# Optimization experiments

Measured on AMD Instinct MI355X. Metric: run time of the kernel, lower is better.

Reference implementation:

```python
import jax, jax.numpy as jnp
import numpy as np

B, C, H, W = 8, 256, 128, 128


def setup_inputs() -> dict:
    key = jax.random.key(0)
    ks = jax.random.split(key, 8)
    s = 1.0 / np.sqrt(C)
    return {
        "edge_feature": jax.random.normal(ks[0], (B, C, H, W), jnp.float32),
        "mask_feature": jax.random.normal(ks[1], (B, C, H, W), jnp.float32),
        # 1x1 conv weights [out_dim, in_dim] + biases
        "Wq": jax.random.normal(ks[2], (C, C), jnp.float32) * s,
        "bq": jax.random.normal(ks[3], (C,), jnp.float32) * 0.01,
        "Wk": jax.random.normal(ks[4], (C, C), jnp.float32) * s,
        "bk": jax.random.normal(ks[5], (C,), jnp.float32) * 0.01,
        "Wv": jax.random.normal(ks[6], (C, C), jnp.float32) * s,
        "bv": jax.random.normal(ks[7], (C,), jnp.float32) * 0.01,
        # torch initializes gamma=0; use 0.5 so the attention path is exercised
        "gamma": jnp.array(0.5, jnp.float32),
    }


def _conv1x1(x, w, b):
    # x: [B,C,H,W], w: [O,C] -> [B,O,H,W]
    return jnp.einsum('oc,bchw->bohw', w, x) + b[None, :, None, None]


def reference(edge_feature, mask_feature, Wq, bq, Wk, bk, Wv, bv, gamma):
    b, c, h, w = edge_feature.shape
    q = _conv1x1(edge_feature, Wq, bq)
    k = _conv1x1(edge_feature, Wk, bk)
    v = _conv1x1(mask_feature, Wv, bv)

    # Criss-cross energies (note: source forward does NOT apply the INF diag mask)
    energy_H = jnp.einsum('bchw,bcjw->bhwj', q, k)  # [B,H,W,H] column attention
    energy_W = jnp.einsum('bchw,bchj->bhwj', q, k)  # [B,H,W,W] row attention

    att = jax.nn.softmax(jnp.concatenate([energy_H, energy_W], axis=3), axis=3)
    att_H4 = att[..., :h]   # [B,H,W,H]
    att_W4 = att[..., h:]   # [B,H,W,W]

    out_H = jnp.einsum('bcjw,bhwj->bchw', v, att_H4)
    out_W = jnp.einsum('bchj,bhwj->bchw', v, att_W4)
    out = gamma * (out_H + out_W) + mask_feature

    # Match torch's returned attention layouts: [B*W,H,H] and [B*H,W,W]
    att_H = jnp.transpose(att_H4, (0, 2, 1, 3)).reshape(b * w, h, h)
    att_W = att_W4.reshape(b * h, w, w)
    return (out, att_H, att_W)
```

## Files before the change

### kernel.cpp

```cpp
#include <hip/hip_runtime.h>

typedef unsigned short u16;
typedef unsigned int   u32;
typedef __attribute__((ext_vector_type(8))) short short8;
typedef __attribute__((ext_vector_type(4))) float f32x4;

#define HW_   16384
constexpr long CHW_ = 4194304L;
constexpr long NT   = 33554432L;

#define GLDS(g, l) __builtin_amdgcn_global_load_lds( \
    (const __attribute__((address_space(1))) void*)(g), \
    (__attribute__((address_space(3))) void*)(l), 16, 0, 0)

__device__ inline u16 f2bf(float x){ u32 u = __float_as_uint(x); u += 0x7fff + ((u>>16)&1); return (u16)(u>>16); }
__device__ inline float bf2f(u16 h){ return __uint_as_float(((u32)h)<<16); }

__device__ inline const short8* frg(const u16* T, int r, int c){
  return (const short8*)(T + r*64 + ((c ^ (r&7))<<3));
}


template<int MODE>
__global__ __launch_bounds__(256) void gemm_nt(
    const char* __restrict__ Aq, const char* __restrict__ Bq,
    const float* __restrict__ bias, const float* __restrict__ gammap,
    float* __restrict__ outFa, float* __restrict__ outFb,
    u16* __restrict__ outUa, u16* __restrict__ outUb)
{
  constexpr int NTl = (MODE <= 1) ? 8 : (MODE == 2 ? 4 : 2);
  __shared__ __align__(16) u16 smem[34048];

  const int t    = threadIdx.x;
  const int lane = t & 63;
  const int wid  = t >> 6;
  const int wr   = (wid >> 1) << 6;
  const int wc   = (wid & 1) << 6;

  long abase = 0, bbase = 0, ars = 0, brs = 0;
  int b = 0, m0 = 0, n0 = 0, xx = 0, ct = 0, dir = 0, sOut = 0;

  if constexpr (MODE == 0) {
    b = blockIdx.z; m0 = blockIdx.x << 7; n0 = blockIdx.y << 7;
    abase = ((long)b * HW_ + m0) * 1024; ars = 1024;
    bbase = (long)n0 * 1024;             brs = 1024;
  } else if constexpr (MODE == 1) {
    int bid = blockIdx.x;
    b = bid >> 8; dir = (bid >> 7) & 1; xx = bid & 127;
    sOut = b * 128 + xx;
    if (dir) { abase = (long)b * 16777216L + (long)xx * 1024; ars = 131072; }
    else     { abase = (long)b * 16777216L + (long)xx * 131072; ars = 1024; }
    bbase = abase; brs = ars;
  } else if constexpr (MODE == 2) {
    b = blockIdx.z; m0 = blockIdx.y << 7; n0 = blockIdx.x << 7;
    abase = (long)m0 * 512;              ars = 512;
    bbase = ((long)b * HW_ + n0) * 512;  brs = 512;
  } else {
    int s = blockIdx.x; ct = blockIdx.y; b = s >> 7; xx = s & 127;
    sOut = s;
    abase = ((long)b * 256 + (long)(ct << 7)) * 32768L + (long)xx * 256; ars = 32768;
    bbase = (long)s * 32768L; brs = 256;
  }

  const char* pA = Aq + abase;
  const char* pB = Bq + bbase;

  f32x4 acc[4][4];
  for (int i = 0; i < 4; i++)
    for (int j = 0; j < 4; j++)
      acc[i][j] = (f32x4){0.f, 0.f, 0.f, 0.f};

  auto stage = [&](int buf, int kt) {
    u16* T1 = smem + buf * 17024;
    u16* T2 = T1 + 8192;
    const long ko = (long)kt * 128;
    #pragma unroll
    for (int i = 0; i < 4; i++) {
      int r = (i << 5) + (t >> 3);
      int c = (t & 7) ^ (r & 7);
      GLDS(pA + (long)r * ars + ko + (c << 4), T1 + (i << 11) + ((t >> 6) << 9));
      GLDS(pB + (long)r * brs + ko + (c << 4), T2 + (i << 11) + ((t >> 6) << 9));
    }
  };

  const int khi = lane >> 4;
  const int rl  = lane & 15;

  stage(0, 0);
  stage(1, 1);

  #pragma unroll
  for (int kt = 0; kt < NTl; ++kt) {
    if (kt + 1 < NTl) asm volatile("s_waitcnt vmcnt(8)" ::: "memory");
    else              asm volatile("s_waitcnt vmcnt(0)" ::: "memory");
    __builtin_amdgcn_sched_barrier(0);
    __builtin_amdgcn_s_barrier();
    __builtin_amdgcn_sched_barrier(0);

    const u16* T1 = smem + (kt & 1) * 17024;
    const u16* T2 = T1 + 8192;

    short8 fa0[4], fa1[4], fb0[4], fb1[4];
    #pragma unroll
    for (int f = 0; f < 4; f++) {
      fa0[f] = *frg(T1, wr + f * 16 + rl, khi);
      fa1[f] = *frg(T1, wr + f * 16 + rl, 4 + khi);
      fb0[f] = *frg(T2, wc + f * 16 + rl, khi);
      fb1[f] = *frg(T2, wc + f * 16 + rl, 4 + khi);
    }

    __builtin_amdgcn_s_setprio(1);
    #pragma unroll
    for (int fm = 0; fm < 4; fm++) {
      #pragma unroll
      for (int fn = 0; fn < 4; fn++) {
        if constexpr (MODE <= 1) {
          acc[fm][fn] = __builtin_amdgcn_mfma_f32_16x16x32_bf16(fa0[fm], fb0[fn], acc[fm][fn], 0, 0, 0);
          acc[fm][fn] = __builtin_amdgcn_mfma_f32_16x16x32_bf16(fa0[fm], fb1[fn], acc[fm][fn], 0, 0, 0);
          acc[fm][fn] = __builtin_amdgcn_mfma_f32_16x16x32_bf16(fa1[fm], fb0[fn], acc[fm][fn], 0, 0, 0);
        } else {
          acc[fm][fn] = __builtin_amdgcn_mfma_f32_16x16x32_bf16(fa0[fm], fb0[fn], acc[fm][fn], 0, 0, 0);
          acc[fm][fn] = __builtin_amdgcn_mfma_f32_16x16x32_bf16(fa1[fm], fb1[fn], acc[fm][fn], 0, 0, 0);
        }
      }
    }
    __builtin_amdgcn_s_setprio(0);

    __builtin_amdgcn_s_barrier();
    __builtin_amdgcn_sched_barrier(0);
    if (kt + 2 < NTl) stage(kt & 1, kt + 2);
  }

  float gma = 0.f;
  if constexpr (MODE == 3) gma = gammap[0];
  float* LDSE = (float*)smem;

  #pragma unroll
  for (int fm = 0; fm < 4; fm++) {
    #pragma unroll
    for (int fn = 0; fn < 4; fn++) {
      #pragma unroll
      for (int r = 0; r < 4; r++) {
        int lr = wr + fm * 16 + ((lane >> 4) << 2) + r;
        int lc = wc + fn * 16 + rl;
        float v = acc[fm][fn][r];
        if constexpr (MODE == 0) v += bias[n0 + lc];
        if constexpr (MODE == 2) v += bias[m0 + lr];
        if constexpr (MODE == 3) v *= gma;
        LDSE[lr * 132 + lc] = v;
      }
    }
  }
  __syncthreads();

  if constexpr (MODE == 0) {
    u16* outp = (n0 < 256) ? outUa : outUb;
    long rowb = ((long)b * HW_ + m0) * 512;
    int cbu = (n0 & 255) * 2;
    #pragma unroll
    for (int k = 0; k < 16; ++k) {
      int row = k * 8 + (t >> 5);
      int iu  = (t & 31) * 8;
      int off = iu & 63;
      int lcol = (iu >> 6) * 32 + (off & 31);
      const float* src = &LDSE[row * 132 + lcol];
      u16 o[8];
      if (off < 32) {
        #pragma unroll
        for (int j = 0; j < 8; j++) o[j] = f2bf(src[j]);
      } else {
        #pragma unroll
        for (int j = 0; j < 8; j++) { float v = src[j]; u16 h = f2bf(v); o[j] = f2bf(v - bf2f(h)); }
      }
      *(short8*)(outp + rowb + (long)row * 512 + cbu + iu) = *(short8*)o;
    }
  } else if constexpr (MODE == 1) {
    float* op = dir ? outFb : outFa;
    long ob = (long)sOut * 16384;
    #pragma unroll
    for (int k = 0; k < 16; ++k) {
      int row = k * 8 + (t >> 5);
      int c4 = (t & 31) * 4;
      f32x4 v = *(const f32x4*)&LDSE[row * 132 + c4];
      *(f32x4*)(op + ob + (long)row * 128 + c4) = v;
    }
  } else {
    #pragma unroll
    for (int k = 0; k < 8; ++k) {
      int row = k * 16 + (t >> 4);
      int c8 = (t & 15) * 8;
      const float* src = &LDSE[row * 132 + c8];
      u16 o[8];
      #pragma unroll
      for (int j = 0; j < 8; j++) o[j] = f2bf(src[j]);
      long addr;
      if constexpr (MODE == 2) addr = ((long)b * 256 + m0 + row) * HW_ + n0 + c8;
      else                     addr = ((long)b * 256 + (ct << 7) + row) * HW_ + (long)xx * 128 + c8;
      *(short8*)(outUa + addr) = *(short8*)o;
    }
  }
}

__global__ __launch_bounds__(256) void split_transpose2(const float* __restrict__ edge,
    const float* __restrict__ mask, u16* __restrict__ Xs, u16* __restrict__ Mt)
{
  int b = blockIdx.z, c0 = blockIdx.y << 5, p0 = blockIdx.x << 5;
  __shared__ float tileE[32][33];
  __shared__ float tileM[32][33];
  int tx = threadIdx.x, ty = threadIdx.y;
  const float* E = edge + (long)b * CHW_;
  const float* M = mask + (long)b * CHW_;
  #pragma unroll
  for (int r = 0; r < 4; r++) {
    int cc = ty + (r << 3);
    long g = (long)(c0 + cc) * HW_ + p0 + tx;
    tileE[cc][tx] = E[g];
    tileM[cc][tx] = M[g];
  }
  __syncthreads();
  int blk = (c0 >> 5) * 64;
  #pragma unroll
  for (int r = 0; r < 4; r++) {
    int pp = ty + (r << 3);
    long prow = (long)b * HW_ + p0 + pp;
    float x = tileE[tx][pp];
    u16 h = f2bf(x);
    Xs[prow * 512 + blk + tx]      = h;
    Xs[prow * 512 + blk + 32 + tx] = f2bf(x - bf2f(h));
    Mt[prow * 256 + c0 + tx]       = f2bf(tileM[tx][pp]);
  }
}

__global__ __launch_bounds__(256) void wsplit(const float* __restrict__ Wq,
    const float* __restrict__ Wk, const float* __restrict__ Wv,
    const float* __restrict__ bq, const float* __restrict__ bk,
    u16* Wc, u16* Wvp, float* bcat)
{
  int i = blockIdx.x * 256 + threadIdx.x;
  int o = i >> 8, c = i & 255;
  long pos = (long)o * 512 + (c >> 5) * 64 + (c & 31);
  float q = Wq[i]; u16 a = f2bf(q); Wc[pos] = a; Wc[pos + 32] = f2bf(q - bf2f(a));
  float k = Wk[i]; u16 d = f2bf(k);
  Wc[pos + 131072] = d; Wc[pos + 131072 + 32] = f2bf(k - bf2f(d));
  Wvp[i] = f2bf(Wv[i]);
  if (blockIdx.x == 0) {
    bcat[threadIdx.x]       = bq[threadIdx.x];
    bcat[256 + threadIdx.x] = bk[threadIdx.x];
  }
}

__global__ __launch_bounds__(256) void transpose_hw_bf16(const u16* __restrict__ src,
                                                         u16* __restrict__ dst)
{
  int bc = blockIdx.z;
  int h0 = blockIdx.x << 5, w0 = blockIdx.y << 5;
  long base = (long)bc * HW_;
  __shared__ u16 tile[32][34];
  int tx = threadIdx.x, ty = threadIdx.y;
  #pragma unroll
  for (int r = 0; r < 4; r++)
    tile[ty + (r << 3)][tx] = src[base + (long)(h0 + ty + (r << 3)) * 128 + w0 + tx];
  __syncthreads();
  #pragma unroll
  for (int r = 0; r < 4; r++) {
    int ww = ty + (r << 3);
    dst[base + (long)(w0 + ww) * 128 + h0 + tx] = tile[tx][ww];
  }
}

__global__ __launch_bounds__(256) void softmax_kernel(float* __restrict__ attH,
    float* __restrict__ attW, u16* __restrict__ aHb, u16* __restrict__ aWb)
{
  int g  = threadIdx.x & 31;
  long r = (long)blockIdx.x * 8 + (threadIdx.x >> 5);
  int b = (int)(r >> 14);
  int h = (int)((r >> 7) & 127);
  int w = (int)(r & 127);
  long baseH = ((long)(b * 128 + w) * 128 + h) * 128;
  long baseW = r * 128;
  float* rp = (g < 16) ? (attH + baseH) : (attW + baseW);
  u16*   up = (g < 16) ? (aHb + baseH)  : (aWb + baseW);
  int j0 = (g & 15) * 8;
  f32x4 v0 = *(f32x4*)(rp + j0);
  f32x4 v1 = *(f32x4*)(rp + j0 + 4);
  float m = fmaxf(fmaxf(fmaxf(v0.x, v0.y), fmaxf(v0.z, v0.w)),
                  fmaxf(fmaxf(v1.x, v1.y), fmaxf(v1.z, v1.w)));
  #pragma unroll
  for (int off = 16; off; off >>= 1) m = fmaxf(m, __shfl_xor(m, off, 32));
  float e[8];
  e[0]=expf(v0.x-m); e[1]=expf(v0.y-m); e[2]=expf(v0.z-m); e[3]=expf(v0.w-m);
  e[4]=expf(v1.x-m); e[5]=expf(v1.y-m); e[6]=expf(v1.z-m); e[7]=expf(v1.w-m);
  float s = ((e[0]+e[1])+(e[2]+e[3])) + ((e[4]+e[5])+(e[6]+e[7]));
  #pragma unroll
  for (int off = 16; off; off >>= 1) s += __shfl_xor(s, off, 32);
  float inv = 1.0f / s;
  #pragma unroll
  for (int j = 0; j < 8; j++) e[j] *= inv;
  *(f32x4*)(rp + j0)     = (f32x4){e[0], e[1], e[2], e[3]};
  *(f32x4*)(rp + j0 + 4) = (f32x4){e[4], e[5], e[6], e[7]};
  u16 o[8];
  #pragma unroll
  for (int j = 0; j < 8; j++) o[j] = f2bf(e[j]);
  *(short8*)(up + j0) = *(short8*)o;
}

__global__ __launch_bounds__(256) void merge_kernel(const u16* __restrict__ tmp,
    const u16* __restrict__ pW, const float* __restrict__ mask, float* __restrict__ out)
{
  int bc = blockIdx.z;
  int h0 = blockIdx.x << 5, w0 = blockIdx.y << 5;
  long base = (long)bc * HW_;
  __shared__ u16 tile[32][33];
  int tx = threadIdx.x, ty = threadIdx.y;
  #pragma unroll
  for (int r = 0; r < 4; r++) {
    int ww = ty + (r << 3);
    tile[ww][tx] = tmp[base + (long)(w0 + ww) * 128 + h0 + tx];
  }
  __syncthreads();
  #pragma unroll
  for (int r = 0; r < 4; r++) {
    int hh = ty + (r << 3);
    long o = base + (long)(h0 + hh) * 128 + w0 + tx;
    out[o] = bf2f(pW[o]) + bf2f(tile[tx][hh]) + mask[o];
  }
}

extern "C" void kernel_launch(void* const* d_in, const int* in_sizes, int n_in,
                              void* d_out, int out_size, void* d_ws, size_t ws_size,
                              hipStream_t stream) {
  const float* edge  = (const float*)d_in[0];
  const float* mask  = (const float*)d_in[1];
  const float* Wq    = (const float*)d_in[2];
  const float* bq    = (const float*)d_in[3];
  const float* Wk    = (const float*)d_in[4];
  const float* bk    = (const float*)d_in[5];
  const float* Wv    = (const float*)d_in[6];
  const float* bv    = (const float*)d_in[7];
  const float* gamma = (const float*)d_in[8];

  float* out  = (float*)d_out;
  float* attH = out + NT;
  float* attW = attH + 16777216L;

  char* W = (char*)d_ws;
  u16* Xs  = (u16*)(W);
  u16* Mt  = (u16*)(W + 134217728L);
  u16* Qs  = (u16*)(W + 201326592L);
  u16* Ks  = (u16*)(W + 335544320L);
  u16* Vb  = (u16*)(W + 469762048L);
  u16* Wc  = (u16*)(W + 536870912L);
  u16* Wvp = Wc + 262144;
  float* bcat = (float*)(Wvp + 65536);
  u16* Vtb = (u16*)(W);
  u16* aWb = (u16*)(W + 67108864L);
  u16* aHb = (u16*)(W + 100663296L);
  u16* tmp = (u16*)(W + 201326592L);
  u16* pW  = (u16*)(W + 335544320L);

  dim3 tb(32, 8);

  wsplit<<<256, 256, 0, stream>>>(Wq, Wk, Wv, bq, bk, Wc, Wvp, bcat);
  split_transpose2<<<dim3(512, 8, 8), tb, 0, stream>>>(edge, mask, Xs, Mt);

  gemm_nt<0><<<dim3(128, 4, 8), 256, 0, stream>>>(
      (const char*)Xs, (const char*)Wc, bcat, nullptr, nullptr, nullptr, Qs, Ks);
  gemm_nt<2><<<dim3(128, 2, 8), 256, 0, stream>>>(
      (const char*)Wvp, (const char*)Mt, bv, nullptr, nullptr, nullptr, Vb, nullptr);

  transpose_hw_bf16<<<dim3(4, 4, 2048), tb, 0, stream>>>(Vb, Vtb);

  gemm_nt<1><<<dim3(2048), 256, 0, stream>>>(
      (const char*)Qs, (const char*)Ks, nullptr, nullptr, attW, attH, nullptr, nullptr);

  softmax_kernel<<<dim3(16384), 256, 0, stream>>>(attH, attW, aHb, aWb);

  gemm_nt<3><<<dim3(1024, 2), 256, 0, stream>>>(
      (const char*)Vtb, (const char*)aHb, nullptr, gamma, nullptr, nullptr, tmp, nullptr);
  gemm_nt<3><<<dim3(1024, 2), 256, 0, stream>>>(
      (const char*)Vb, (const char*)aWb, nullptr, gamma, nullptr, nullptr, pW, nullptr);

  merge_kernel<<<dim3(4, 4, 2048), tb, 0, stream>>>(tmp, pW, mask, out);
}
```

Measured before the change: 634.3 us.

## Vectorize input split-transpose, merge MODE3 GEMM launches, use nontemporal stores

Rewrites the split/transpose of edge and mask so each block loads a full 256-channel slab with 16-byte vector loads and writes whole 64/32-element bf16 rows with 16-byte stores, replacing scattered 2-byte stores. Fuses the two MODE3 attention-value GEMMs into one launch, using blockIdx.z to choose the operands and output. Switches the softmax fp32 attention writes and the final output writes to nontemporal stores to reduce cache pollution. The new transpose uses large per-thread register arrays and about 66KB of LDS per block, which may lower occupancy.

```diff
diff --git a/kernel.cpp b/kernel.cpp
--- a/kernel.cpp
+++ b/kernel.cpp
@@ -24,6 +24,7 @@
 template<int MODE>
 __global__ __launch_bounds__(256) void gemm_nt(
     const char* __restrict__ Aq, const char* __restrict__ Bq,
+    const char* __restrict__ Aq2, const char* __restrict__ Bq2,
     const float* __restrict__ bias, const float* __restrict__ gammap,
     float* __restrict__ outFa, float* __restrict__ outFb,
     u16* __restrict__ outUa, u16* __restrict__ outUb)
@@ -39,6 +40,9 @@
 
   long abase = 0, bbase = 0, ars = 0, brs = 0;
   int b = 0, m0 = 0, n0 = 0, xx = 0, ct = 0, dir = 0, sOut = 0;
+  const char* Ause = Aq;
+  const char* Buse = Bq;
+  u16* outU = outUa;
 
   if constexpr (MODE == 0) {
     b = blockIdx.z; m0 = blockIdx.x << 7; n0 = blockIdx.y << 7;
@@ -58,12 +62,13 @@
   } else {
     int s = blockIdx.x; ct = blockIdx.y; b = s >> 7; xx = s & 127;
     sOut = s;
+    if (blockIdx.z) { Ause = Aq2; Buse = Bq2; outU = outUb; }
     abase = ((long)b * 256 + (long)(ct << 7)) * 32768L + (long)xx * 256; ars = 32768;
     bbase = (long)s * 32768L; brs = 256;
   }
 
-  const char* pA = Aq + abase;
-  const char* pB = Bq + bbase;
+  const char* pA = Ause + abase;
+  const char* pB = Buse + bbase;
 
   f32x4 acc[4][4];
   for (int i = 0; i < 4; i++)
@@ -196,7 +201,7 @@
       long addr;
       if constexpr (MODE == 2) addr = ((long)b * 256 + m0 + row) * HW_ + n0 + c8;
       else                     addr = ((long)b * 256 + (ct << 7) + row) * HW_ + (long)xx * 128 + c8;
-      *(short8*)(outUa + addr) = *(short8*)o;
+      *(short8*)(outU + addr) = *(short8*)o;
     }
   }
 }
@@ -204,31 +209,42 @@
 __global__ __launch_bounds__(256) void split_transpose2(const float* __restrict__ edge,
     const float* __restrict__ mask, u16* __restrict__ Xs, u16* __restrict__ Mt)
 {
-  int b = blockIdx.z, c0 = blockIdx.y << 5, p0 = blockIdx.x << 5;
-  __shared__ float tileE[32][33];
-  __shared__ float tileM[32][33];
-  int tx = threadIdx.x, ty = threadIdx.y;
-  const float* E = edge + (long)b * CHW_;
-  const float* M = mask + (long)b * CHW_;
-  #pragma unroll
-  for (int r = 0; r < 4; r++) {
-    int cc = ty + (r << 3);
-    long g = (long)(c0 + cc) * HW_ + p0 + tx;
-    tileE[cc][tx] = E[g];
-    tileM[cc][tx] = M[g];
+  int b = blockIdx.z, p0 = blockIdx.x << 5;
+  __shared__ float El[32][260];
+  __shared__ float Ml[32][260];
+  int t = threadIdx.x;
+  const float* E = edge + (long)b * CHW_ + (long)t * HW_ + p0;
+  const float* M = mask + (long)b * CHW_ + (long)t * HW_ + p0;
+  #pragma unroll
+  for (int i = 0; i < 8; i++) {
+    f32x4 ve = *(const f32x4*)(E + i * 4);
+    f32x4 vm = *(const f32x4*)(M + i * 4);
+    #pragma unroll
+    for (int k = 0; k < 4; k++) {
+      El[i * 4 + k][t] = ve[k];
+      Ml[i * 4 + k][t] = vm[k];
+    }
   }
   __syncthreads();
-  int blk = (c0 >> 5) * 64;
-  #pragma unroll
-  for (int r = 0; r < 4; r++) {
-    int pp = ty + (r << 3);
-    long prow = (long)b * HW_ + p0 + pp;
-    float x = tileE[tx][pp];
+  int r = t >> 3, s = t & 7;
+  long prow = (long)b * HW_ + p0 + r;
+  u16 ob[64];
+  u16 mb[32];
+  #pragma unroll
+  for (int i = 0; i < 32; i++) {
+    int cc = (i + s) & 31;
+    float x = El[r][s * 32 + cc];
     u16 h = f2bf(x);
-    Xs[prow * 512 + blk + tx]      = h;
-    Xs[prow * 512 + blk + 32 + tx] = f2bf(x - bf2f(h));
-    Mt[prow * 256 + c0 + tx]       = f2bf(tileM[tx][pp]);
-  }
+    ob[cc]      = h;
+    ob[32 + cc] = f2bf(x - bf2f(h));
+    mb[cc]      = f2bf(Ml[r][s * 32 + cc]);
+  }
+  u16* xo = Xs + prow * 512 + s * 64;
+  #pragma unroll
+  for (int k = 0; k < 8; k++) *(short8*)(xo + k * 8) = *(short8*)(ob + k * 8);
+  u16* mo = Mt + prow * 256 + s * 32;
+  #pragma unroll
+  for (int k = 0; k < 4; k++) *(short8*)(mo + k * 8) = *(short8*)(mb + k * 8);
 }
 
 __global__ __launch_bounds__(256) void wsplit(const float* __restrict__ Wq,
@@ -296,8 +312,8 @@
   float inv = 1.0f / s;
   #pragma unroll
   for (int j = 0; j < 8; j++) e[j] *= inv;
-  *(f32x4*)(rp + j0)     = (f32x4){e[0], e[1], e[2], e[3]};
-  *(f32x4*)(rp + j0 + 4) = (f32x4){e[4], e[5], e[6], e[7]};
+  __builtin_nontemporal_store((f32x4){e[0], e[1], e[2], e[3]}, (f32x4*)(rp + j0));
+  __builtin_nontemporal_store((f32x4){e[4], e[5], e[6], e[7]}, (f32x4*)(rp + j0 + 4));
   u16 o[8];
   #pragma unroll
   for (int j = 0; j < 8; j++) o[j] = f2bf(e[j]);
@@ -322,7 +338,8 @@
   for (int r = 0; r < 4; r++) {
     int hh = ty + (r << 3);
     long o = base + (long)(h0 + hh) * 128 + w0 + tx;
-    out[o] = bf2f(pW[o]) + bf2f(tile[tx][hh]) + mask[o];
+    float v = bf2f(pW[o]) + bf2f(tile[tx][hh]) + mask[o];
+    __builtin_nontemporal_store(v, out + o);
   }
 }
 
@@ -361,24 +378,26 @@
   dim3 tb(32, 8);
 
   wsplit<<<256, 256, 0, stream>>>(Wq, Wk, Wv, bq, bk, Wc, Wvp, bcat);
-  split_transpose2<<<dim3(512, 8, 8), tb, 0, stream>>>(edge, mask, Xs, Mt);
+  split_transpose2<<<dim3(512, 1, 8), 256, 0, stream>>>(edge, mask, Xs, Mt);
 
   gemm_nt<0><<<dim3(128, 4, 8), 256, 0, stream>>>(
-      (const char*)Xs, (const char*)Wc, bcat, nullptr, nullptr, nullptr, Qs, Ks);
+      (const char*)Xs, (const char*)Wc, nullptr, nullptr, bcat, nullptr,
+      nullptr, nullptr, Qs, Ks);
   gemm_nt<2><<<dim3(128, 2, 8), 256, 0, stream>>>(
-      (const char*)Wvp, (const char*)Mt, bv, nullptr, nullptr, nullptr, Vb, nullptr);
+      (const char*)Wvp, (const char*)Mt, nullptr, nullptr, bv, nullptr,
+      nullptr, nullptr, Vb, nullptr);
 
   transpose_hw_bf16<<<dim3(4, 4, 2048), tb, 0, stream>>>(Vb, Vtb);
 
   gemm_nt<1><<<dim3(2048), 256, 0, stream>>>(
-      (const char*)Qs, (const char*)Ks, nullptr, nullptr, attW, attH, nullptr, nullptr);
+      (const char*)Qs, (const char*)Ks, nullptr, nullptr, nullptr, nullptr,
+      attW, attH, nullptr, nullptr);
 
   softmax_kernel<<<dim3(16384), 256, 0, stream>>>(attH, attW, aHb, aWb);
 
-  gemm_nt<3><<<dim3(1024, 2), 256, 0, stream>>>(
-      (const char*)Vtb, (const char*)aHb, nullptr, gamma, nullptr, nullptr, tmp, nullptr);
-  gemm_nt<3><<<dim3(1024, 2), 256, 0, stream>>>(
-      (const char*)Vb, (const char*)aWb, nullptr, gamma, nullptr, nullptr, pW, nullptr);
+  gemm_nt<3><<<dim3(1024, 2, 2), 256, 0, stream>>>(
+      (const char*)Vtb, (const char*)aHb, (const char*)Vb, (const char*)aWb,
+      nullptr, gamma, nullptr, nullptr, tmp, pW);
 
   merge_kernel<<<dim3(4, 4, 2048), tb, 0, stream>>>(tmp, pW, mask, out);
 }
```

After: 951.9 us. 50.1% more time.
